# Optimization experiments

Hardware: AMD Instinct MI355X
Metric: run time of the kernel (lower is better)

The kernel has to match this reference:

```python
import jax, jax.numpy as jnp
import numpy as np

H = 512          # num_hiddens
HEADS = 2
DH = H // HEADS
B, S, T = 64, 1024, 64


def setup_inputs() -> dict:
    key = jax.random.key(0)
    ks = jax.random.split(key, 13)
    sc = 0.02
    return {
        "X": jax.random.normal(ks[0], (B, T), jnp.float32),
        "enc_outputs": jax.random.normal(ks[1], (B, S, H), jnp.float32),
        "hidden_state": jax.random.normal(ks[2], (1, B, H), jnp.float32),
        "Wq": jax.random.normal(ks[3], (H, H), jnp.float32) * sc,
        "Wk": jax.random.normal(ks[4], (H, H), jnp.float32) * sc,
        "Wv": jax.random.normal(ks[5], (H, H), jnp.float32) * sc,
        "Wo": jax.random.normal(ks[6], (H, H), jnp.float32) * sc,
        "w_ih": jax.random.normal(ks[7], (3 * H, H + 1), jnp.float32) * sc,
        "w_hh": jax.random.normal(ks[8], (3 * H, H), jnp.float32) * sc,
        "b_ih": jnp.zeros((3 * H,), jnp.float32),
        "b_hh": jnp.zeros((3 * H,), jnp.float32),
        "Wd": jax.random.normal(ks[9], (1, H), jnp.float32) * sc,
        "bd": jnp.zeros((1,), jnp.float32),
    }


def reference(X, enc_outputs, hidden_state, Wq, Wk, Wv, Wo,
              w_ih, w_hh, b_ih, b_hh, Wd, bd):
    # Pre-project keys/values once (enc_outputs is constant across steps).
    K = (enc_outputs @ Wk.T).reshape(B, S, HEADS, DH)
    V = (enc_outputs @ Wv.T).reshape(B, S, HEADS, DH)
    scale = 1.0 / jnp.sqrt(jnp.asarray(DH, jnp.float32))

    def step(h, x_t):
        # h: (B, H) last-layer hidden; x_t: (B,) scalar decoder input
        q = (h @ Wq.T).reshape(B, HEADS, DH)
        scores = jnp.einsum('bhd,bshd->bhs', q, K) * scale
        attn = jax.nn.softmax(scores, axis=-1)
        ctx = jnp.einsum('bhs,bshd->bhd', attn, V).reshape(B, H) @ Wo.T
        xin = jnp.concatenate([ctx, x_t[:, None]], axis=-1)  # (B, H+1)
        gi = xin @ w_ih.T + b_ih
        gh = h @ w_hh.T + b_hh
        ir, iz, inn = jnp.split(gi, 3, axis=-1)
        hr, hz, hn = jnp.split(gh, 3, axis=-1)
        r = jax.nn.sigmoid(ir + hr)
        z = jax.nn.sigmoid(iz + hz)
        n = jnp.tanh(inn + r * hn)
        h_new = (1.0 - z) * n + z * h
        return h_new, h_new

    h0 = hidden_state[-1]                       # num_layers == 1
    h_final, outs = jax.lax.scan(step, h0, X.T)  # outs: (T, B, H)
    outputs = jnp.transpose(outs, (1, 0, 2)) @ Wd.T + bd  # (B, T, 1)
    return outputs, enc_outputs, h_final[None]
```

## Files before the change

### kernel.cpp

```cpp
#include <hip/hip_runtime.h>
#include <hip/hip_fp8.h>
#include <stdint.h>

typedef __attribute__((ext_vector_type(8))) short short8v;
typedef __attribute__((ext_vector_type(4))) float f32x4;

__device__ __forceinline__ float bflo(uint32_t u){ union{uint32_t i; float f;}v; v.i = u<<16; return v.f; }
__device__ __forceinline__ float bfhi(uint32_t u){ union{uint32_t i; float f;}v; v.i = u & 0xffff0000u; return v.f; }
__device__ __forceinline__ uint16_t f2bf(float f){
  union{float f; uint32_t i;}v; v.f = f;
  uint32_t x = v.i;
  x += 0x7fffu + ((x>>16)&1u);
  return (uint16_t)(x>>16);
}
__device__ __forceinline__ uint8_t f2fp8(float f){
  return __builtin_bit_cast(uint8_t, __hip_fp8_e4m3(f));
}
__device__ __forceinline__ float fp82f(uint8_t b){
  return (float)__builtin_bit_cast(__hip_fp8_e4m3, b);
}

__global__ void prep_kernel(const float* __restrict__ hidden, const float* __restrict__ w_ih,
                            const float* __restrict__ w_hh, const float* __restrict__ Wo,
                            float* __restrict__ y, float* __restrict__ h0,
                            uint16_t* __restrict__ wihp, uint16_t* __restrict__ whhb,
                            uint16_t* __restrict__ wob){
  int idx = blockIdx.x*blockDim.x + threadIdx.x;
  int n = gridDim.x*blockDim.x;
  for (int i=idx; i<4096; i+=n) y[i] = 0.f;
  for (int i=idx; i<32768; i+=n) h0[i] = hidden[i];
  for (int i=idx; i<1536*520; i+=n){
    int j = i/520, c = i - j*520;
    wihp[i] = (c<513) ? f2bf(w_ih[(size_t)j*513 + c]) : (uint16_t)0;
  }
  for (int i=idx; i<1536*512; i+=n) whhb[i] = f2bf(w_hh[i]);
  for (int i=idx; i<512*512; i+=n)  wob[i]  = f2bf(Wo[i]);
}

__global__ void copy_enc_kernel(const float4* __restrict__ src, float4* __restrict__ dst, int n4){
  int idx = blockIdx.x*blockDim.x + threadIdx.x;
  int stride = gridDim.x*blockDim.x;
  for (int i=idx; i<n4; i+=stride) dst[i] = src[i];
}

__global__ __launch_bounds__(256) void kv_build_kernel(
    const float* __restrict__ enc, const float* __restrict__ Wk, const float* __restrict__ Wv,
    uint8_t* __restrict__ Kf, uint8_t* __restrict__ Vf)
{
  __shared__ uint16_t As[128][40];
  __shared__ uint16_t Bs[128][40];
  const int s0 = blockIdx.x*128;
  const int d0 = blockIdx.y*128;
  const int z  = blockIdx.z;
  const int b  = z>>1;
  const float* __restrict__ W = (z&1) ? Wv : Wk;
  uint8_t* __restrict__ On    = (z&1) ? Vf : Kf;
  const int tid = threadIdx.x;
  const int wv = tid>>6, lane = tid&63;
  const int r = tid>>1, hh = (tid&1)*16;
  const float* encb = enc + (size_t)b*1024*512;

  f32x4 acc[2][8];
  #pragma unroll
  for (int i=0;i<2;++i)
    #pragma unroll
    for (int j=0;j<8;++j) acc[i][j] = (f32x4){0.f,0.f,0.f,0.f};

  const int fr = lane&15, kq = (lane>>4)*8;

  for (int k0=0;k0<512;k0+=32){
    const float4* sa = (const float4*)(encb + (size_t)(s0+r)*512 + k0 + hh);
    const float4* sb = (const float4*)(W    + (size_t)(d0+r)*512 + k0 + hh);
    float4 va[4], vb[4];
    #pragma unroll
    for (int q=0;q<4;++q){ va[q]=sa[q]; vb[q]=sb[q]; }
    __syncthreads();
    uint16_t* pa = &As[r][hh];
    uint16_t* pb = &Bs[r][hh];
    #pragma unroll
    for (int q=0;q<4;++q){
      pa[4*q+0]=f2bf(va[q].x); pa[4*q+1]=f2bf(va[q].y); pa[4*q+2]=f2bf(va[q].z); pa[4*q+3]=f2bf(va[q].w);
      pb[4*q+0]=f2bf(vb[q].x); pb[4*q+1]=f2bf(vb[q].y); pb[4*q+2]=f2bf(vb[q].z); pb[4*q+3]=f2bf(vb[q].w);
    }
    __syncthreads();
    short8v af[2], bfr[8];
    af[0] = *(const short8v*)&As[wv*32 +      fr][kq];
    af[1] = *(const short8v*)&As[wv*32 + 16 + fr][kq];
    #pragma unroll
    for (int n2=0;n2<8;++n2) bfr[n2] = *(const short8v*)&Bs[n2*16 + fr][kq];
    #pragma unroll
    for (int mi=0;mi<2;++mi)
      #pragma unroll
      for (int n2=0;n2<8;++n2)
        acc[mi][n2] = __builtin_amdgcn_mfma_f32_16x16x32_bf16(af[mi], bfr[n2], acc[mi][n2], 0,0,0);
  }
  const int rq = (lane>>4)*4;
  #pragma unroll
  for (int mi=0;mi<2;++mi){
    #pragma unroll
    for (int reg=0; reg<4; ++reg){
      int s = s0 + wv*32 + mi*16 + rq + reg;
      #pragma unroll
      for (int n2=0;n2<8;++n2){
        int d = d0 + n2*16 + fr;
        int head = d>>8, dh = d&255;
        On[(((size_t)b*2+head)*1024 + s)*256 + dh] = f2fp8(acc[mi][n2][reg]);
      }
    }
  }
}

__global__ __launch_bounds__(512) void attn_kernel(
    const uint8_t* __restrict__ Kf, const uint8_t* __restrict__ Vf,
    const float* __restrict__ h_in, const float* __restrict__ Wq,
    float* __restrict__ ctxp, float* __restrict__ ml)
{
  const int ch = blockIdx.x, head = blockIdx.y, b = blockIdx.z;
  const int tid = threadIdx.x;
  __shared__ float h_s[512];
  __shared__ float q_s[256];
  __shared__ float p_s[512];
  __shared__ float cpa[2048];
  __shared__ float red[17];
  h_s[tid] = h_in[b*512 + tid];
  __syncthreads();
  {
    int d = tid>>1, hf = tid&1;
    const float4* wr = (const float4*)(Wq + (size_t)(head*256+d)*512 + hf*256);
    const float* hb = h_s + hf*256;
    float s = 0.f;
    #pragma unroll 8
    for (int i=0;i<64;++i){
      float4 w = wr[i];
      s = fmaf(w.x, hb[4*i+0], s); s = fmaf(w.y, hb[4*i+1], s);
      s = fmaf(w.z, hb[4*i+2], s); s = fmaf(w.w, hb[4*i+3], s);
    }
    s += __shfl_xor(s, 1);
    if (hf==0) q_s[d] = s * 0.0625f;
  }
  __syncthreads();
  const uint8_t* Kb = Kf + ((size_t)(b*2+head)*1024 + ch*512)*256;
  {
    int qd = tid&3, rbase = tid>>2;
    for (int p=0;p<4;++p){
      int r = p*128 + rbase;
      const uint4* Kr = (const uint4*)(Kb + (size_t)r*256);
      float s=0.f;
      #pragma unroll
      for (int u=0;u<4;++u){
        uint4 v = Kr[qd + 4*u];
        const float* qq = q_s + (qd+4*u)*16;
        uint32_t w;
        w = v.x;
        s = fmaf(fp82f(w&255), qq[0], s);  s = fmaf(fp82f((w>>8)&255), qq[1], s);
        s = fmaf(fp82f((w>>16)&255), qq[2], s); s = fmaf(fp82f(w>>24), qq[3], s);
        w = v.y;
        s = fmaf(fp82f(w&255), qq[4], s);  s = fmaf(fp82f((w>>8)&255), qq[5], s);
        s = fmaf(fp82f((w>>16)&255), qq[6], s); s = fmaf(fp82f(w>>24), qq[7], s);
        w = v.z;
        s = fmaf(fp82f(w&255), qq[8], s);  s = fmaf(fp82f((w>>8)&255), qq[9], s);
        s = fmaf(fp82f((w>>16)&255), qq[10], s); s = fmaf(fp82f(w>>24), qq[11], s);
        w = v.w;
        s = fmaf(fp82f(w&255), qq[12], s); s = fmaf(fp82f((w>>8)&255), qq[13], s);
        s = fmaf(fp82f((w>>16)&255), qq[14], s); s = fmaf(fp82f(w>>24), qq[15], s);
      }
      s += __shfl_xor(s,1); s += __shfl_xor(s,2);
      if (qd==0) p_s[r] = s;
    }
  }
  __syncthreads();
  float sc = p_s[tid];
  float m;
  {
    float v = sc;
    #pragma unroll
    for (int o=32;o;o>>=1) v = fmaxf(v, __shfl_xor(v,o));
    if ((tid&63)==0) red[tid>>6] = v;
    __syncthreads();
    if (tid==0){ float mm=red[0]; for(int i=1;i<8;++i) mm=fmaxf(mm,red[i]); red[16]=mm; }
    __syncthreads();
    m = red[16];
  }
  float pv = __expf(sc - m);
  float l;
  {
    float v = pv;
    #pragma unroll
    for (int o=32;o;o>>=1) v += __shfl_xor(v,o);
    if ((tid&63)==0) red[8+(tid>>6)] = v;
    __syncthreads();
    if (tid==0){ float ss=0.f; for(int i=0;i<8;++i) ss+=red[8+i]; red[16]=ss; }
    __syncthreads();
    l = red[16];
  }
  p_s[tid] = pv;
  __syncthreads();
  const uint8_t* Vb = Vf + ((size_t)(b*2+head)*1024 + ch*512)*256;
  {
    int d4 = (tid&63)*4, sh = tid>>6;
    float a0=0,a1=0,a2=0,a3=0;
    for (int s2=sh*64; s2<sh*64+64; ++s2){
      float pw = p_s[s2];
      uint32_t v = *(const uint32_t*)(Vb + (size_t)s2*256 + d4);
      a0 = fmaf(pw, fp82f(v&255), a0);       a1 = fmaf(pw, fp82f((v>>8)&255), a1);
      a2 = fmaf(pw, fp82f((v>>16)&255), a2); a3 = fmaf(pw, fp82f(v>>24), a3);
    }
    cpa[sh*256 + d4+0]=a0; cpa[sh*256 + d4+1]=a1;
    cpa[sh*256 + d4+2]=a2; cpa[sh*256 + d4+3]=a3;
  }
  __syncthreads();
  if (tid<256){
    float s=0.f;
    #pragma unroll
    for (int sh=0;sh<8;++sh) s += cpa[sh*256 + tid];
    ctxp[((size_t)(b*2+head)*2 + ch)*256 + tid] = s;
  }
  if (tid==0){
    size_t mb = ((size_t)(b*2+head)*2 + ch)*2;
    ml[mb] = m; ml[mb+1] = l;
  }
}

__global__ __launch_bounds__(256) void ctxo_kernel(
    const float* __restrict__ ctxp, const float* __restrict__ ml,
    const float* __restrict__ X, const uint16_t* __restrict__ wob,
    float* __restrict__ xin, int t)
{
  const int b = blockIdx.x; const int tid = threadIdx.x;
  __shared__ float ctx_s[512];
  #pragma unroll
  for (int head=0; head<2; ++head){
    size_t base = (size_t)(b*2+head)*2;
    float m0 = ml[base*2+0], l0 = ml[base*2+1];
    float m1 = ml[base*2+2], l1 = ml[base*2+3];
    float mm = fmaxf(m0,m1);
    float w0 = __expf(m0-mm), w1 = __expf(m1-mm);
    float linv = 1.f/(w0*l0 + w1*l1);
    float c0 = ctxp[base*256 + tid];
    float c1 = ctxp[(base+1)*256 + tid];
    ctx_s[head*256+tid] = (w0*c0 + w1*c1)*linv;
  }
  __syncthreads();
  for (int j=tid; j<512; j+=256){
    const uint4* wr = (const uint4*)(wob + (size_t)j*512);
    float s=0.f;
    #pragma unroll 4
    for (int i=0;i<64;++i){
      uint4 w = wr[i];
      s = fmaf(bflo(w.x), ctx_s[8*i+0], s); s = fmaf(bfhi(w.x), ctx_s[8*i+1], s);
      s = fmaf(bflo(w.y), ctx_s[8*i+2], s); s = fmaf(bfhi(w.y), ctx_s[8*i+3], s);
      s = fmaf(bflo(w.z), ctx_s[8*i+4], s); s = fmaf(bfhi(w.z), ctx_s[8*i+5], s);
      s = fmaf(bflo(w.w), ctx_s[8*i+6], s); s = fmaf(bfhi(w.w), ctx_s[8*i+7], s);
    }
    xin[(size_t)b*516 + j] = s;
  }
  if (tid==0){
    xin[(size_t)b*516+512] = X[b*64 + t];
    xin[(size_t)b*516+513] = 0.f; xin[(size_t)b*516+514] = 0.f; xin[(size_t)b*516+515] = 0.f;
  }
}

__global__ __launch_bounds__(256) void gru_kernel(
    const float* __restrict__ xin_g, const float* __restrict__ h_in, float* __restrict__ h_out,
    const uint16_t* __restrict__ wihp, const uint16_t* __restrict__ whhb,
    const float* __restrict__ b_ih, const float* __restrict__ b_hh,
    const float* __restrict__ Wd, const float* __restrict__ bd,
    float* __restrict__ y, int t)
{
  const int j0 = blockIdx.x*64, b0 = blockIdx.y*4;
  const int tid = threadIdx.x;
  __shared__ float xin_s[4][520];
  __shared__ float h_s[4][512];
  for (int bb2=0; bb2<4; ++bb2){
    for (int c2=tid; c2<520; c2+=256) xin_s[bb2][c2] = (c2<516) ? xin_g[(size_t)(b0+bb2)*516 + c2] : 0.f;
    for (int c2=tid; c2<512; c2+=256) h_s[bb2][c2]   = h_in[(size_t)(b0+bb2)*512 + c2];
  }
  __syncthreads();
  const int bb = tid>>6, jj = tid&63;
  const int j = j0 + jj, b = b0 + bb;
  const float* xs = xin_s[bb];
  const float* hs = h_s[bb];
  float gi[3], gh[3];
  #pragma unroll
  for (int g=0; g<3; ++g){
    const uint4* wr = (const uint4*)(wihp + (size_t)(g*512 + j)*520);
    float s = 0.f;
    #pragma unroll 5
    for (int i=0;i<65;++i){
      uint4 w = wr[i];
      s = fmaf(bflo(w.x), xs[8*i+0], s); s = fmaf(bfhi(w.x), xs[8*i+1], s);
      s = fmaf(bflo(w.y), xs[8*i+2], s); s = fmaf(bfhi(w.y), xs[8*i+3], s);
      s = fmaf(bflo(w.z), xs[8*i+4], s); s = fmaf(bfhi(w.z), xs[8*i+5], s);
      s = fmaf(bflo(w.w), xs[8*i+6], s); s = fmaf(bfhi(w.w), xs[8*i+7], s);
    }
    gi[g] = s + b_ih[g*512 + j];
    const uint4* wh = (const uint4*)(whhb + (size_t)(g*512 + j)*512);
    float sh = 0.f;
    #pragma unroll 4
    for (int i=0;i<64;++i){
      uint4 w = wh[i];
      sh = fmaf(bflo(w.x), hs[8*i+0], sh); sh = fmaf(bfhi(w.x), hs[8*i+1], sh);
      sh = fmaf(bflo(w.y), hs[8*i+2], sh); sh = fmaf(bfhi(w.y), hs[8*i+3], sh);
      sh = fmaf(bflo(w.z), hs[8*i+4], sh); sh = fmaf(bfhi(w.z), hs[8*i+5], sh);
      sh = fmaf(bflo(w.w), hs[8*i+6], sh); sh = fmaf(bfhi(w.w), hs[8*i+7], sh);
    }
    gh[g] = sh + b_hh[g*512 + j];
  }
  float r = 1.f/(1.f + __expf(-(gi[0]+gh[0])));
  float z = 1.f/(1.f + __expf(-(gi[1]+gh[1])));
  float n = tanhf(gi[2] + r*gh[2]);
  float hn = (1.f - z)*n + z*hs[j];
  h_out[(size_t)b*512 + j] = hn;
  float part = hn * Wd[j];
  #pragma unroll
  for (int o=32;o>=1;o>>=1) part += __shfl_xor(part, o);
  if (jj==0){
    float add = part + ((blockIdx.x==0) ? bd[0] : 0.f);
    atomicAdd(y + b*64 + t, add);
  }
}

__global__ void fin_kernel(const float* __restrict__ hfin, float* __restrict__ dst){
  int i = blockIdx.x*blockDim.x + threadIdx.x;
  if (i < 32768) dst[i] = hfin[i];
}

extern "C" void kernel_launch(void* const* d_in, const int* in_sizes, int n_in,
                              void* d_out, int out_size, void* d_ws, size_t ws_size,
                              hipStream_t stream)
{
  const float* X    = (const float*)d_in[0];
  const float* enc  = (const float*)d_in[1];
  const float* hid  = (const float*)d_in[2];
  const float* Wq   = (const float*)d_in[3];
  const float* Wk   = (const float*)d_in[4];
  const float* Wv   = (const float*)d_in[5];
  const float* Wo   = (const float*)d_in[6];
  const float* w_ih = (const float*)d_in[7];
  const float* w_hh = (const float*)d_in[8];
  const float* b_ih = (const float*)d_in[9];
  const float* b_hh = (const float*)d_in[10];
  const float* Wd   = (const float*)d_in[11];
  const float* bd   = (const float*)d_in[12];
  float* out = (float*)d_out;

  uint8_t* Kf = (uint8_t*)(out + 4096);
  uint8_t* Vf = Kf + 33554432;

  char* ws = (char*)d_ws;
  float*    h0   = (float*)(ws + 0);
  float*    h1   = (float*)(ws + 131072);
  float*    cp   = (float*)(ws + 262144);
  float*    ml   = (float*)(ws + 524288);
  uint16_t* wihp = (uint16_t*)(ws + 528384);
  uint16_t* whhb = (uint16_t*)(ws + 2125824);
  uint16_t* wob  = (uint16_t*)(ws + 3698688);
  float*    xin  = (float*)(ws + 4222976);

  prep_kernel<<<dim3(512), dim3(256), 0, stream>>>(hid, w_ih, w_hh, Wo, out, h0, wihp, whhb, wob);
  kv_build_kernel<<<dim3(8,4,128), dim3(256), 0, stream>>>(enc, Wk, Wv, Kf, Vf);

  float* hb[2] = {h0, h1};
  for (int t=0; t<64; ++t){
    const float* hi = hb[t&1];
    float* ho = hb[1-(t&1)];
    attn_kernel<<<dim3(2,2,64), dim3(512), 0, stream>>>(Kf, Vf, hi, Wq, cp, ml);
    ctxo_kernel<<<dim3(64), dim3(256), 0, stream>>>(cp, ml, X, wob, xin, t);
    gru_kernel<<<dim3(8,16), dim3(256), 0, stream>>>(xin, hi, ho, wihp, whhb, b_ih, b_hh, Wd, bd, out, t);
  }
  copy_enc_kernel<<<dim3(4096), dim3(256), 0, stream>>>((const float4*)enc, (float4*)(out + 4096), 8388608);
  fin_kernel<<<dim3(128), dim3(256), 0, stream>>>(h0, out + 4096 + 33554432);
}
```

Baseline: 8.519 ms.

## Fuse per-step attention, output projection and GRU into one kernel per batch

Three per-timestep launches (attention, context/Wo projection, GRU) become a single 1024-thread block per batch element that runs both heads of attention, the Wo projection, the GRU gates and the output dot product. Intermediate buffers in global memory, the split-softmax merge and the atomicAdd go away. Weights are now stored as fp16, Wq included, and the matvecs use packed fdot2. Only 64 blocks are launched, each re-streaming about 5 MB of fp16 weights, so the GPU is underused and weight bandwidth per block may become the limit. fp16 also adds precision risk.

Measured after the change: 9.835 ms. +15.4%, slower.

```diff
diff --git a/kernel.cpp b/kernel.cpp
--- a/kernel.cpp
+++ b/kernel.cpp
@@ -4,9 +4,8 @@
 
 typedef __attribute__((ext_vector_type(8))) short short8v;
 typedef __attribute__((ext_vector_type(4))) float f32x4;
-
-__device__ __forceinline__ float bflo(uint32_t u){ union{uint32_t i; float f;}v; v.i = u<<16; return v.f; }
-__device__ __forceinline__ float bfhi(uint32_t u){ union{uint32_t i; float f;}v; v.i = u & 0xffff0000u; return v.f; }
+typedef _Float16 h2 __attribute__((ext_vector_type(2)));
+
 __device__ __forceinline__ uint16_t f2bf(float f){
   union{float f; uint32_t i;}v; v.f = f;
   uint32_t x = v.i;
@@ -19,22 +18,32 @@
 __device__ __forceinline__ float fp82f(uint8_t b){
   return (float)__builtin_bit_cast(__hip_fp8_e4m3, b);
 }
-
-__global__ void prep_kernel(const float* __restrict__ hidden, const float* __restrict__ w_ih,
-                            const float* __restrict__ w_hh, const float* __restrict__ Wo,
+__device__ __forceinline__ h2 as_h2(uint32_t u){ return __builtin_bit_cast(h2, u); }
+__device__ __forceinline__ float dot2(h2 a, h2 b, float c){
+#if __has_builtin(__builtin_amdgcn_fdot2)
+  return __builtin_amdgcn_fdot2(a, b, c, false);
+#else
+  return c + (float)a[0]*(float)b[0] + (float)a[1]*(float)b[1];
+#endif
+}
+
+__global__ void prep_kernel(const float* __restrict__ hidden,
+                            const float* __restrict__ Wq, const float* __restrict__ Wo,
+                            const float* __restrict__ w_ih, const float* __restrict__ w_hh,
                             float* __restrict__ y, float* __restrict__ h0,
-                            uint16_t* __restrict__ wihp, uint16_t* __restrict__ whhb,
-                            uint16_t* __restrict__ wob){
+                            _Float16* __restrict__ wq_h, _Float16* __restrict__ wo_h,
+                            _Float16* __restrict__ wih_h, _Float16* __restrict__ whh_h){
   int idx = blockIdx.x*blockDim.x + threadIdx.x;
   int n = gridDim.x*blockDim.x;
   for (int i=idx; i<4096; i+=n) y[i] = 0.f;
   for (int i=idx; i<32768; i+=n) h0[i] = hidden[i];
-  for (int i=idx; i<1536*520; i+=n){
-    int j = i/520, c = i - j*520;
-    wihp[i] = (c<513) ? f2bf(w_ih[(size_t)j*513 + c]) : (uint16_t)0;
-  }
-  for (int i=idx; i<1536*512; i+=n) whhb[i] = f2bf(w_hh[i]);
-  for (int i=idx; i<512*512; i+=n)  wob[i]  = f2bf(Wo[i]);
+  for (int i=idx; i<262144; i+=n) wq_h[i] = (_Float16)Wq[i];
+  for (int i=idx; i<262144; i+=n) wo_h[i] = (_Float16)Wo[i];
+  for (int i=idx; i<1536*544; i+=n){
+    int j = i/544, c = i - j*544;
+    wih_h[i] = (c<513) ? (_Float16)w_ih[(size_t)j*513 + c] : (_Float16)0.f;
+  }
+  for (int i=idx; i<1536*512; i+=n) whh_h[i] = (_Float16)w_hh[i];
 }
 
 __global__ void copy_enc_kernel(const float4* __restrict__ src, float4* __restrict__ dst, int n4){
@@ -110,46 +119,64 @@
   }
 }
 
-__global__ __launch_bounds__(512) void attn_kernel(
+__global__ __launch_bounds__(1024) void step_kernel(
     const uint8_t* __restrict__ Kf, const uint8_t* __restrict__ Vf,
-    const float* __restrict__ h_in, const float* __restrict__ Wq,
-    float* __restrict__ ctxp, float* __restrict__ ml)
+    const float* __restrict__ h_in, float* __restrict__ h_out,
+    const _Float16* __restrict__ wq_h, const _Float16* __restrict__ wo_h,
+    const _Float16* __restrict__ wih_h, const _Float16* __restrict__ whh_h,
+    const float* __restrict__ b_ih, const float* __restrict__ b_hh,
+    const float* __restrict__ Wd, const float* __restrict__ bd,
+    const float* __restrict__ X, float* __restrict__ y, int t)
 {
-  const int ch = blockIdx.x, head = blockIdx.y, b = blockIdx.z;
-  const int tid = threadIdx.x;
+  const int b = blockIdx.x, tid = threadIdx.x;
+  const int lane = tid&63, wid = tid>>6;
   __shared__ float h_s[512];
-  __shared__ float q_s[256];
-  __shared__ float p_s[512];
-  __shared__ float cpa[2048];
-  __shared__ float red[17];
-  h_s[tid] = h_in[b*512 + tid];
-  __syncthreads();
-  {
-    int d = tid>>1, hf = tid&1;
-    const float4* wr = (const float4*)(Wq + (size_t)(head*256+d)*512 + hf*256);
-    const float* hb = h_s + hf*256;
-    float s = 0.f;
+  __shared__ __align__(16) h2 hh_s[256];
+  __shared__ float q_s[512];
+  __shared__ float p_s[2][1024];
+  __shared__ float red[40];
+  __shared__ float cpa[8][512];
+  __shared__ float ctx_f[512];
+  __shared__ __align__(16) h2 ctx_h[256];
+  __shared__ __align__(16) _Float16 xin_half[544];
+
+  if (tid<256){
+    float2 hv = ((const float2*)(h_in + (size_t)b*512))[tid];
+    h_s[2*tid]=hv.x; h_s[2*tid+1]=hv.y;
+    hh_s[tid] = (h2){(_Float16)hv.x, (_Float16)hv.y};
+  }
+  __syncthreads();
+
+  {
+    int o = tid>>1, hf = tid&1;
+    const uint4* wr = ((const uint4*)(wq_h + (size_t)o*512)) + hf*32;
+    const uint4* hp = ((const uint4*)hh_s) + hf*32;
+    float s=0.f;
     #pragma unroll 8
-    for (int i=0;i<64;++i){
-      float4 w = wr[i];
-      s = fmaf(w.x, hb[4*i+0], s); s = fmaf(w.y, hb[4*i+1], s);
-      s = fmaf(w.z, hb[4*i+2], s); s = fmaf(w.w, hb[4*i+3], s);
-    }
-    s += __shfl_xor(s, 1);
-    if (hf==0) q_s[d] = s * 0.0625f;
-  }
-  __syncthreads();
-  const uint8_t* Kb = Kf + ((size_t)(b*2+head)*1024 + ch*512)*256;
-  {
-    int qd = tid&3, rbase = tid>>2;
-    for (int p=0;p<4;++p){
-      int r = p*128 + rbase;
-      const uint4* Kr = (const uint4*)(Kb + (size_t)r*256);
+    for (int i=0;i<32;++i){
+      uint4 w = wr[i], hv = hp[i];
+      s = dot2(as_h2(w.x), as_h2(hv.x), s);
+      s = dot2(as_h2(w.y), as_h2(hv.y), s);
+      s = dot2(as_h2(w.z), as_h2(hv.z), s);
+      s = dot2(as_h2(w.w), as_h2(hv.w), s);
+    }
+    s += __shfl_xor(s,1);
+    if (hf==0) q_s[o] = s*0.0625f;
+  }
+  __syncthreads();
+
+  {
+    int qd = tid&3, rb2 = tid>>2;
+    #pragma unroll
+    for (int p=0;p<8;++p){
+      int r2 = p*256 + rb2;
+      int head = r2>>10, s2 = r2&1023;
+      const uint4* Kr = (const uint4*)(Kf + (((size_t)b*2+head)*1024 + s2)*256);
       float s=0.f;
       #pragma unroll
       for (int u=0;u<4;++u){
-        uint4 v = Kr[qd + 4*u];
-        const float* qq = q_s + (qd+4*u)*16;
+        uint4 v = Kr[qd+4*u];
+        const float* qq = q_s + head*256 + (qd+4*u)*16;
         uint32_t w;
         w = v.x;
         s = fmaf(fp82f(w&255), qq[0], s);  s = fmaf(fp82f((w>>8)&255), qq[1], s);
@@ -165,158 +192,141 @@
         s = fmaf(fp82f((w>>16)&255), qq[14], s); s = fmaf(fp82f(w>>24), qq[15], s);
       }
       s += __shfl_xor(s,1); s += __shfl_xor(s,2);
-      if (qd==0) p_s[r] = s;
-    }
-  }
-  __syncthreads();
-  float sc = p_s[tid];
-  float m;
-  {
-    float v = sc;
-    #pragma unroll
-    for (int o=32;o;o>>=1) v = fmaxf(v, __shfl_xor(v,o));
-    if ((tid&63)==0) red[tid>>6] = v;
-    __syncthreads();
-    if (tid==0){ float mm=red[0]; for(int i=1;i<8;++i) mm=fmaxf(mm,red[i]); red[16]=mm; }
-    __syncthreads();
-    m = red[16];
-  }
-  float pv = __expf(sc - m);
-  float l;
-  {
-    float v = pv;
-    #pragma unroll
-    for (int o=32;o;o>>=1) v += __shfl_xor(v,o);
-    if ((tid&63)==0) red[8+(tid>>6)] = v;
-    __syncthreads();
-    if (tid==0){ float ss=0.f; for(int i=0;i<8;++i) ss+=red[8+i]; red[16]=ss; }
-    __syncthreads();
-    l = red[16];
-  }
-  p_s[tid] = pv;
-  __syncthreads();
-  const uint8_t* Vb = Vf + ((size_t)(b*2+head)*1024 + ch*512)*256;
-  {
-    int d4 = (tid&63)*4, sh = tid>>6;
-    float a0=0,a1=0,a2=0,a3=0;
-    for (int s2=sh*64; s2<sh*64+64; ++s2){
-      float pw = p_s[s2];
-      uint32_t v = *(const uint32_t*)(Vb + (size_t)s2*256 + d4);
-      a0 = fmaf(pw, fp82f(v&255), a0);       a1 = fmaf(pw, fp82f((v>>8)&255), a1);
-      a2 = fmaf(pw, fp82f((v>>16)&255), a2); a3 = fmaf(pw, fp82f(v>>24), a3);
-    }
-    cpa[sh*256 + d4+0]=a0; cpa[sh*256 + d4+1]=a1;
-    cpa[sh*256 + d4+2]=a2; cpa[sh*256 + d4+3]=a3;
-  }
-  __syncthreads();
-  if (tid<256){
+      if (qd==0) p_s[head][s2] = s;
+    }
+  }
+  __syncthreads();
+
+  float a0 = p_s[0][tid], a1 = p_s[1][tid];
+  {
+    float v0=a0, v1=a1;
+    #pragma unroll
+    for (int o=32;o;o>>=1){ v0=fmaxf(v0,__shfl_xor(v0,o)); v1=fmaxf(v1,__shfl_xor(v1,o)); }
+    if (lane==0){ red[wid]=v0; red[16+wid]=v1; }
+  }
+  __syncthreads();
+  if (tid==0){
+    float m0=red[0], m1=red[16];
+    for (int i=1;i<16;++i){ m0=fmaxf(m0,red[i]); m1=fmaxf(m1,red[16+i]); }
+    red[32]=m0; red[33]=m1;
+  }
+  __syncthreads();
+  float e0 = __expf(a0-red[32]), e1 = __expf(a1-red[33]);
+  p_s[0][tid]=e0; p_s[1][tid]=e1;
+  {
+    float v0=e0, v1=e1;
+    #pragma unroll
+    for (int o=32;o;o>>=1){ v0+=__shfl_xor(v0,o); v1+=__shfl_xor(v1,o); }
+    if (lane==0){ red[wid]=v0; red[16+wid]=v1; }
+  }
+  __syncthreads();
+  if (tid==0){
+    float l0=0.f,l1=0.f;
+    for (int i=0;i<16;++i){ l0+=red[i]; l1+=red[16+i]; }
+    red[36]=1.f/l0; red[37]=1.f/l1;
+  }
+  __syncthreads();
+
+  {
+    int u = tid&127, sh = tid>>7;
+    int head = u>>6, d4 = (u&63)*4;
+    const uint8_t* Vb = Vf + (((size_t)b*2+head)*1024 + sh*128)*256 + d4;
+    const float* pp = &p_s[head][sh*128];
+    float c0=0,c1=0,c2=0,c3=0;
+    #pragma unroll 4
+    for (int s2=0;s2<128;++s2){
+      float pw = pp[s2];
+      uint32_t v = *(const uint32_t*)(Vb + (size_t)s2*256);
+      c0 = fmaf(pw, fp82f(v&255), c0);
+      c1 = fmaf(pw, fp82f((v>>8)&255), c1);
+      c2 = fmaf(pw, fp82f((v>>16)&255), c2);
+      c3 = fmaf(pw, fp82f(v>>24), c3);
+    }
+    int ob = head*256 + d4;
+    cpa[sh][ob]=c0; cpa[sh][ob+1]=c1; cpa[sh][ob+2]=c2; cpa[sh][ob+3]=c3;
+  }
+  __syncthreads();
+  if (tid<512){
     float s=0.f;
     #pragma unroll
-    for (int sh=0;sh<8;++sh) s += cpa[sh*256 + tid];
-    ctxp[((size_t)(b*2+head)*2 + ch)*256 + tid] = s;
-  }
+    for (int sh=0;sh<8;++sh) s += cpa[sh][tid];
+    ctx_f[tid] = s * red[36 + (tid>>8)];
+  }
+  __syncthreads();
+  if (tid<256) ctx_h[tid] = (h2){(_Float16)ctx_f[2*tid], (_Float16)ctx_f[2*tid+1]};
+  __syncthreads();
+
+  {
+    int j = tid>>1, hf = tid&1;
+    const uint4* wr = ((const uint4*)(wo_h + (size_t)j*512)) + hf*32;
+    const uint4* cp4 = ((const uint4*)ctx_h) + hf*32;
+    float s=0.f;
+    #pragma unroll 8
+    for (int i=0;i<32;++i){
+      uint4 w = wr[i], cv = cp4[i];
+      s = dot2(as_h2(w.x), as_h2(cv.x), s);
+      s = dot2(as_h2(w.y), as_h2(cv.y), s);
+      s = dot2(as_h2(w.z), as_h2(cv.z), s);
+      s = dot2(as_h2(w.w), as_h2(cv.w), s);
+    }
+    s += __shfl_xor(s,1);
+    if (hf==0) xin_half[j] = (_Float16)s;
+  }
+  if (tid>=512 && tid<544) xin_half[tid] = (tid==512) ? (_Float16)X[(size_t)b*64+t] : (_Float16)0.f;
+  __syncthreads();
+
+  {
+    int ks = tid&1, j = tid>>1;
+    float g6[6];
+    #pragma unroll
+    for (int g=0; g<3; ++g){
+      const uint4* wr = ((const uint4*)(wih_h + (size_t)(g*512+j)*544)) + ks*34;
+      const uint4* xp = ((const uint4*)xin_half) + ks*34;
+      float s=0.f;
+      #pragma unroll 2
+      for (int i=0;i<34;++i){
+        uint4 w = wr[i], xv = xp[i];
+        s = dot2(as_h2(w.x), as_h2(xv.x), s);
+        s = dot2(as_h2(w.y), as_h2(xv.y), s);
+        s = dot2(as_h2(w.z), as_h2(xv.z), s);
+        s = dot2(as_h2(w.w), as_h2(xv.w), s);
+      }
+      g6[g]=s;
+      const uint4* wh = ((const uint4*)(whh_h + (size_t)(g*512+j)*512)) + ks*32;
+      const uint4* hp = ((const uint4*)hh_s) + ks*32;
+      float s2=0.f;
+      #pragma unroll 2
+      for (int i=0;i<32;++i){
+        uint4 w = wh[i], hv = hp[i];
+        s2 = dot2(as_h2(w.x), as_h2(hv.x), s2);
+        s2 = dot2(as_h2(w.y), as_h2(hv.y), s2);
+        s2 = dot2(as_h2(w.z), as_h2(hv.z), s2);
+        s2 = dot2(as_h2(w.w), as_h2(hv.w), s2);
+      }
+      g6[3+g]=s2;
+    }
+    #pragma unroll
+    for (int i2=0;i2<6;++i2) g6[i2] += __shfl_xor(g6[i2],1);
+    float part = 0.f;
+    if (ks==0){
+      float gi0=g6[0]+b_ih[j], gi1=g6[1]+b_ih[512+j], gi2=g6[2]+b_ih[1024+j];
+      float gh0=g6[3]+b_hh[j], gh1=g6[4]+b_hh[512+j], gh2=g6[5]+b_hh[1024+j];
+      float r = 1.f/(1.f+__expf(-(gi0+gh0)));
+      float z = 1.f/(1.f+__expf(-(gi1+gh1)));
+      float n = tanhf(gi2 + r*gh2);
+      float hn = (1.f-z)*n + z*h_s[j];
+      h_out[(size_t)b*512+j] = hn;
+      part = hn*Wd[j];
+    }
+    #pragma unroll
+    for (int o=32;o;o>>=1) part += __shfl_xor(part,o);
+    if (lane==0) red[wid] = part;
+  }
+  __syncthreads();
   if (tid==0){
-    size_t mb = ((size_t)(b*2+head)*2 + ch)*2;
-    ml[mb] = m; ml[mb+1] = l;
-  }
-}
-
-__global__ __launch_bounds__(256) void ctxo_kernel(
-    const float* __restrict__ ctxp, const float* __restrict__ ml,
-    const float* __restrict__ X, const uint16_t* __restrict__ wob,
-    float* __restrict__ xin, int t)
-{
-  const int b = blockIdx.x; const int tid = threadIdx.x;
-  __shared__ float ctx_s[512];
-  #pragma unroll
-  for (int head=0; head<2; ++head){
-    size_t base = (size_t)(b*2+head)*2;
-    float m0 = ml[base*2+0], l0 = ml[base*2+1];
-    float m1 = ml[base*2+2], l1 = ml[base*2+3];
-    float mm = fmaxf(m0,m1);
-    float w0 = __expf(m0-mm), w1 = __expf(m1-mm);
-    float linv = 1.f/(w0*l0 + w1*l1);
-    float c0 = ctxp[base*256 + tid];
-    float c1 = ctxp[(base+1)*256 + tid];
-    ctx_s[head*256+tid] = (w0*c0 + w1*c1)*linv;
-  }
-  __syncthreads();
-  for (int j=tid; j<512; j+=256){
-    const uint4* wr = (const uint4*)(wob + (size_t)j*512);
-    float s=0.f;
-    #pragma unroll 4
-    for (int i=0;i<64;++i){
-      uint4 w = wr[i];
-      s = fmaf(bflo(w.x), ctx_s[8*i+0], s); s = fmaf(bfhi(w.x), ctx_s[8*i+1], s);
-      s = fmaf(bflo(w.y), ctx_s[8*i+2], s); s = fmaf(bfhi(w.y), ctx_s[8*i+3], s);
-      s = fmaf(bflo(w.z), ctx_s[8*i+4], s); s = fmaf(bfhi(w.z), ctx_s[8*i+5], s);
-      s = fmaf(bflo(w.w), ctx_s[8*i+6], s); s = fmaf(bfhi(w.w), ctx_s[8*i+7], s);
-    }
-    xin[(size_t)b*516 + j] = s;
-  }
-  if (tid==0){
-    xin[(size_t)b*516+512] = X[b*64 + t];
-    xin[(size_t)b*516+513] = 0.f; xin[(size_t)b*516+514] = 0.f; xin[(size_t)b*516+515] = 0.f;
-  }
-}
-
-__global__ __launch_bounds__(256) void gru_kernel(
-    const float* __restrict__ xin_g, const float* __restrict__ h_in, float* __restrict__ h_out,
-    const uint16_t* __restrict__ wihp, const uint16_t* __restrict__ whhb,
-    const float* __restrict__ b_ih, const float* __restrict__ b_hh,
-    const float* __restrict__ Wd, const float* __restrict__ bd,
-    float* __restrict__ y, int t)
-{
-  const int j0 = blockIdx.x*64, b0 = blockIdx.y*4;
-  const int tid = threadIdx.x;
-  __shared__ float xin_s[4][520];
-  __shared__ float h_s[4][512];
-  for (int bb2=0; bb2<4; ++bb2){
-    for (int c2=tid; c2<520; c2+=256) xin_s[bb2][c2] = (c2<516) ? xin_g[(size_t)(b0+bb2)*516 + c2] : 0.f;
-    for (int c2=tid; c2<512; c2+=256) h_s[bb2][c2]   = h_in[(size_t)(b0+bb2)*512 + c2];
-  }
-  __syncthreads();
-  const int bb = tid>>6, jj = tid&63;
-  const int j = j0 + jj, b = b0 + bb;
-  const float* xs = xin_s[bb];
-  const float* hs = h_s[bb];
-  float gi[3], gh[3];
-  #pragma unroll
-  for (int g=0; g<3; ++g){
-    const uint4* wr = (const uint4*)(wihp + (size_t)(g*512 + j)*520);
-    float s = 0.f;
-    #pragma unroll 5
-    for (int i=0;i<65;++i){
-      uint4 w = wr[i];
-      s = fmaf(bflo(w.x), xs[8*i+0], s); s = fmaf(bfhi(w.x), xs[8*i+1], s);
-      s = fmaf(bflo(w.y), xs[8*i+2], s); s = fmaf(bfhi(w.y), xs[8*i+3], s);
-      s = fmaf(bflo(w.z), xs[8*i+4], s); s = fmaf(bfhi(w.z), xs[8*i+5], s);
-      s = fmaf(bflo(w.w), xs[8*i+6], s); s = fmaf(bfhi(w.w), xs[8*i+7], s);
-    }
-    gi[g] = s + b_ih[g*512 + j];
-    const uint4* wh = (const uint4*)(whhb + (size_t)(g*512 + j)*512);
-    float sh = 0.f;
-    #pragma unroll 4
-    for (int i=0;i<64;++i){
-      uint4 w = wh[i];
-      sh = fmaf(bflo(w.x), hs[8*i+0], sh); sh = fmaf(bfhi(w.x), hs[8*i+1], sh);
-      sh = fmaf(bflo(w.y), hs[8*i+2], sh); sh = fmaf(bfhi(w.y), hs[8*i+3], sh);
-      sh = fmaf(bflo(w.z), hs[8*i+4], sh); sh = fmaf(bfhi(w.z), hs[8*i+5], sh);
-      sh = fmaf(bflo(w.w), hs[8*i+6], sh); sh = fmaf(bfhi(w.w), hs[8*i+7], sh);
-    }
-    gh[g] = sh + b_hh[g*512 + j];
-  }
-  float r = 1.f/(1.f + __expf(-(gi[0]+gh[0])));
-  float z = 1.f/(1.f + __expf(-(gi[1]+gh[1])));
-  float n = tanhf(gi[2] + r*gh[2]);
-  float hn = (1.f - z)*n + z*hs[j];
-  h_out[(size_t)b*512 + j] = hn;
-  float part = hn * Wd[j];
-  #pragma unroll
-  for (int o=32;o>=1;o>>=1) part += __shfl_xor(part, o);
-  if (jj==0){
-    float add = part + ((blockIdx.x==0) ? bd[0] : 0.f);
-    atomicAdd(y + b*64 + t, add);
+    float s = bd[0];
+    for (int i=0;i<16;++i) s += red[i];
+    y[(size_t)b*64+t] = s;
   }
 }
 
@@ -348,25 +358,24 @@
   uint8_t* Vf = Kf + 33554432;
 
   char* ws = (char*)d_ws;
-  float*    h0   = (float*)(ws + 0);
-  float*    h1   = (float*)(ws + 131072);
-  float*    cp   = (float*)(ws + 262144);
-  float*    ml   = (float*)(ws + 524288);
-  uint16_t* wihp = (uint16_t*)(ws + 528384);
-  uint16_t* whhb = (uint16_t*)(ws + 2125824);
-  uint16_t* wob  = (uint16_t*)(ws + 3698688);
-  float*    xin  = (float*)(ws + 4222976);
-
-  prep_kernel<<<dim3(512), dim3(256), 0, stream>>>(hid, w_ih, w_hh, Wo, out, h0, wihp, whhb, wob);
+  float*     h0    = (float*)(ws + 0);
+  float*     h1    = (float*)(ws + 131072);
+  _Float16*  wq_h  = (_Float16*)(ws + 262144);
+  _Float16*  wo_h  = (_Float16*)(ws + 786432);
+  _Float16*  wih_h = (_Float16*)(ws + 1310720);
+  _Float16*  whh_h = (_Float16*)(ws + 2981888);
+
+  prep_kernel<<<dim3(512), dim3(256), 0, stream>>>(hid, Wq, Wo, w_ih, w_hh, out, h0,
+                                                   wq_h, wo_h, wih_h, whh_h);
   kv_build_kernel<<<dim3(8,4,128), dim3(256), 0, stream>>>(enc, Wk, Wv, Kf, Vf);
 
   float* hb[2] = {h0, h1};
   for (int t=0; t<64; ++t){
     const float* hi = hb[t&1];
     float* ho = hb[1-(t&1)];
-    attn_kernel<<<dim3(2,2,64), dim3(512), 0, stream>>>(Kf, Vf, hi, Wq, cp, ml);
-    ctxo_kernel<<<dim3(64), dim3(256), 0, stream>>>(cp, ml, X, wob, xin, t);
-    gru_kernel<<<dim3(8,16), dim3(256), 0, stream>>>(xin, hi, ho, wihp, whhb, b_ih, b_hh, Wd, bd, out, t);
+    step_kernel<<<dim3(64), dim3(1024), 0, stream>>>(Kf, Vf, hi, ho,
+                                                     wq_h, wo_h, wih_h, whh_h,
+                                                     b_ih, b_hh, Wd, bd, X, out, t);
   }
   copy_enc_kernel<<<dim3(4096), dim3(256), 0, stream>>>((const float4*)enc, (float4*)(out + 4096), 8388608);
   fin_kernel<<<dim3(128), dim3(256), 0, stream>>>(h0, out + 4096 + 33554432);
```
